# Kernel optimization log

Hardware: AMD Instinct MI355X
Metric: run time of the kernel (lower is better)

The kernel has to match this reference:

```python
import jax, jax.numpy as jnp
import numpy as np

N = 30000      # nodes
E = 480000     # edges (avg degree 16)
NF = 4         # n_field
NM = 8         # n_meshfield
H = 128        # hidden_size == latent_size
T = 4          # n_time
DEPTH_MID = 8  # depth-2 middle convs per GCNBlock
EPS = 1e-5     # PyG InstanceNorm eps
DT = 5 * (4.0 / 200)  # = 0.1, hard-coded in forward


def _glorot(k, shape):
    fan_in = shape[-2]
    return (jax.random.uniform(k, shape, jnp.float32, -1.0, 1.0) / np.sqrt(fan_in)).astype(jnp.float32)


def setup_inputs() -> dict:
    key = jax.random.key(0)
    ks = jax.random.split(key, 12)
    inp = {}
    inp['F_0'] = jax.random.normal(ks[0], (N, NF), jnp.float32)
    inp['edge_index'] = jax.random.randint(ks[1], (2, E), 0, N)
    inp['meshfield'] = jax.random.normal(ks[2], (N, NM), jnp.float32)
    inp['n_time'] = T
    # mesh_decriptor GCNBlock params (10 GCNConv layers)
    inp['mesh_W0'] = _glorot(ks[3], (NM, H)); inp['mesh_b0'] = jnp.zeros((H,), jnp.float32)
    inp['mesh_Wh'] = _glorot(ks[4], (DEPTH_MID, H, H)); inp['mesh_bh'] = jnp.zeros((DEPTH_MID, H), jnp.float32)
    inp['mesh_W9'] = _glorot(ks[5], (H, H)); inp['mesh_b9'] = jnp.zeros((H,), jnp.float32)
    # differentiator GCNBlock params; input dim = n_field + latent_size
    din = NF + H
    inp['diff_W0'] = _glorot(ks[6], (din, H)); inp['diff_b0'] = jnp.zeros((H,), jnp.float32)
    inp['diff_Wh'] = _glorot(ks[7], (DEPTH_MID, H, H)); inp['diff_bh'] = jnp.zeros((DEPTH_MID, H), jnp.float32)
    inp['diff_W9'] = _glorot(ks[8], (H, NF)); inp['diff_b9'] = jnp.zeros((NF,), jnp.float32)
    return inp


def _gcn_norm(edge_index, n):
    # PyG GCNConv: add self-loops, sym-normalize D^-1/2 (A+I) D^-1/2
    loops = jnp.arange(n)
    row = jnp.concatenate([edge_index[0], loops])
    col = jnp.concatenate([edge_index[1], loops])
    deg = jax.ops.segment_sum(jnp.ones_like(col, jnp.float32), col, num_segments=n)
    dinv = jnp.where(deg > 0, jax.lax.rsqrt(jnp.maximum(deg, 1.0)), 0.0)
    return row, col, dinv[row] * dinv[col]


def _conv(x, W, b, row, col, enorm, n):
    h = x @ W                                   # [n, out]
    m = h[row] * enorm[:, None]                 # gather + edge normalization
    return jax.ops.segment_sum(m, col, num_segments=n) + b  # scatter-add + bias


def _instance_norm(x):
    # single graph, affine=False: per-channel normalize over nodes
    m = x.mean(axis=0)
    v = x.var(axis=0)
    return (x - m) * jax.lax.rsqrt(v + EPS)


def _gcn_block(x, W0, b0, Wh, bh, W9, b9, row, col, enorm, n):
    x = _conv(x, W0, b0, row, col, enorm, n)
    x = _instance_norm(x)
    def body(c, wb):
        W, b = wb
        return _conv(jax.nn.relu(c), W, b, row, col, enorm, n), None
    x, _ = jax.lax.scan(body, x, (Wh, bh))
    return _conv(x, W9, b9, row, col, enorm, n)


def reference(F_0, edge_index, meshfield, n_time,
              mesh_W0, mesh_b0, mesh_Wh, mesh_bh, mesh_W9, mesh_b9,
              diff_W0, diff_b0, diff_Wh, diff_bh, diff_W9, diff_b9):
    n = F_0.shape[0]
    row, col, enorm = _gcn_norm(edge_index, n)
    mesh = jnp.tanh(_gcn_block(meshfield, mesh_W0, mesh_b0, mesh_Wh, mesh_bh,
                               mesh_W9, mesh_b9, row, col, enorm, n))

    def step(F_cur, _):
        x = jnp.concatenate([F_cur, mesh], axis=1)   # [n, n_field + latent]
        F_dot = jnp.tanh(_gcn_block(x, diff_W0, diff_b0, diff_Wh, diff_bh,
                                    diff_W9, diff_b9, row, col, enorm, n))
        F_next = jnp.tanh(F_cur + F_dot * DT)
        # original: F_current = F_next.detach()
        return jax.lax.stop_gradient(F_next), (F_next, F_dot)

    _, (Fs, F_dots) = jax.lax.scan(step, F_0, None, length=n_time)
    # [T, n, f] -> [n, T, f] to match torch.cat(..., dim=1)
    return jnp.transpose(Fs, (1, 0, 2)), jnp.transpose(F_dots, (1, 0, 2))
```

## Files before the change

kernel.cpp:

```cpp
#include <hip/hip_runtime.h>
#include <math.h>

typedef __attribute__((ext_vector_type(8))) short short8;
typedef __attribute__((ext_vector_type(4))) float f32x4;
typedef unsigned int uint;
typedef unsigned short ushort;

__device__ __forceinline__ ushort f2bf(float f) {
  union { float f; uint u; } v; v.f = f;
  uint u = v.u;
  uint r = (u + 0x7FFFu + ((u >> 16) & 1u)) >> 16;
  return (ushort)r;
}
__device__ __forceinline__ float bflo(uint u) { union { uint u; float f; } v; v.u = u << 16; return v.f; }
__device__ __forceinline__ float bfhi(uint u) { union { uint u; float f; } v; v.u = u & 0xFFFF0000u; return v.f; }
__device__ __forceinline__ uint packbf(float a, float b) { return (uint)f2bf(a) | ((uint)f2bf(b) << 16); }


static __global__ void k_count(const int* __restrict__ col, int* __restrict__ cnt, int E) {
  int e = blockIdx.x * blockDim.x + threadIdx.x;
  if (e < E) atomicAdd(&cnt[col[e]], 1);
}

static __global__ void k_dinv(const int* __restrict__ cnt, float* __restrict__ dinv, int N) {
  int v = blockIdx.x * blockDim.x + threadIdx.x;
  if (v < N) dinv[v] = rsqrtf((float)cnt[v] + 1.0f);
}

static __global__ void k_scan(const int* __restrict__ cnt, int* __restrict__ rowptr, int N) {
  __shared__ int buf[1024];
  __shared__ int carry;
  int t = threadIdx.x;
  if (t == 0) carry = 0;
  __syncthreads();
  for (int base = 0; base < N; base += 1024) {
    int i = base + t;
    int x = (i < N) ? cnt[i] : 0;
    buf[t] = x;
    __syncthreads();
    for (int o = 1; o < 1024; o <<= 1) {
      int val = (t >= o) ? buf[t - o] : 0;
      __syncthreads();
      buf[t] += val;
      __syncthreads();
    }
    int inc = buf[t];
    if (i < N) rowptr[i] = carry + inc - x;
    __syncthreads();
    if (t == 1023) carry += inc;
    __syncthreads();
  }
  if (t == 0) rowptr[N] = carry;
}

static __global__ void k_fill(const int* __restrict__ row, const int* __restrict__ col,
                              const float* __restrict__ dinv, const int* __restrict__ rowptr,
                              int* __restrict__ fillc, int* __restrict__ csr_src,
                              float* __restrict__ csr_w, int E) {
  int e = blockIdx.x * blockDim.x + threadIdx.x;
  if (e >= E) return;
  int s = row[e], d = col[e];
  int pos = rowptr[d] + atomicAdd(&fillc[d], 1);
  csr_src[pos] = s;
  csr_w[pos] = dinv[s] * dinv[d];
}


static __global__ void k_wprep(const float* __restrict__ W, ushort* __restrict__ Wt,
                               int K, int Kpad, int Nc) {
  int l = blockIdx.y;
  int idx = blockIdx.x * 256 + threadIdx.x;
  if (idx >= Nc * Kpad) return;
  int n = idx / Kpad, k = idx - n * Kpad;
  const float* Wl = W + (size_t)l * K * Nc;
  ushort* Wtl = Wt + (size_t)l * Nc * Kpad;
  Wtl[idx] = (k < K) ? f2bf(Wl[(size_t)k * Nc + n]) : (ushort)0;
}


static __global__ __launch_bounds__(256) void k_gemm16(
    const ushort* __restrict__ A, const ushort* __restrict__ Bt,
    ushort* __restrict__ Y, int M, int K) {
  __shared__ ushort As[128 * 40];
  __shared__ ushort Bs[128 * 40];
  const int tid = threadIdx.x;
  const int lane = tid & 63;
  const int wave = tid >> 6;
  const int wr = wave >> 1, wc = wave & 1;
  const int bm = blockIdx.x * 128;
  const int l15 = lane & 15, lk = lane >> 4;
  const int r0 = tid >> 2, o0 = tid & 3;

  f32x4 acc[4][4];
#pragma unroll
  for (int i = 0; i < 4; ++i)
#pragma unroll
    for (int j = 0; j < 4; ++j) acc[i][j] = (f32x4){0.f, 0.f, 0.f, 0.f};

  for (int k0 = 0; k0 < K; k0 += 32) {
    short8 a0 = *(const short8*)(A + (size_t)(bm + r0) * K + k0 + o0 * 8);
    short8 a1 = *(const short8*)(A + (size_t)(bm + r0 + 64) * K + k0 + o0 * 8);
    short8 b0 = *(const short8*)(Bt + (size_t)r0 * K + k0 + o0 * 8);
    short8 b1 = *(const short8*)(Bt + (size_t)(r0 + 64) * K + k0 + o0 * 8);
    __syncthreads();
    *(short8*)(As + r0 * 40 + o0 * 8) = a0;
    *(short8*)(As + (r0 + 64) * 40 + o0 * 8) = a1;
    *(short8*)(Bs + r0 * 40 + o0 * 8) = b0;
    *(short8*)(Bs + (r0 + 64) * 40 + o0 * 8) = b1;
    __syncthreads();
    short8 af[4], bfr[4];
#pragma unroll
    for (int i = 0; i < 4; ++i) {
      af[i]  = *(const short8*)(As + (wr * 64 + i * 16 + l15) * 40 + lk * 8);
      bfr[i] = *(const short8*)(Bs + (wc * 64 + i * 16 + l15) * 40 + lk * 8);
    }
#pragma unroll
    for (int i = 0; i < 4; ++i)
#pragma unroll
      for (int j = 0; j < 4; ++j)
        acc[i][j] = __builtin_amdgcn_mfma_f32_16x16x32_bf16(af[i], bfr[j], acc[i][j], 0, 0, 0);
  }
#pragma unroll
  for (int i = 0; i < 4; ++i) {
#pragma unroll
    for (int r = 0; r < 4; ++r) {
      int row = bm + wr * 64 + i * 16 + lk * 4 + r;
      if (row < M) {
#pragma unroll
        for (int j = 0; j < 4; ++j) {
          int col = wc * 64 + j * 16 + l15;
          Y[(size_t)row * 128 + col] = f2bf(acc[i][j][r]);
        }
      }
    }
  }
}


static __global__ __launch_bounds__(256) void k_gemm_small(
    const ushort* __restrict__ A, const float* __restrict__ W, float* __restrict__ Y, int M) {
  __shared__ float Ws[512];
  int tid = threadIdx.x;
  for (int i = tid; i < 512; i += 256) Ws[i] = W[i];
  __syncthreads();
  int m = blockIdx.x * 256 + tid;
  if (m >= M) return;
  const uint* a = (const uint*)(A + (size_t)m * 128);
  float a0 = 0, a1 = 0, a2 = 0, a3 = 0;
#pragma unroll 8
  for (int k2 = 0; k2 < 64; ++k2) {
    uint u = a[k2];
    float x0 = bflo(u), x1 = bfhi(u);
    const float* w = Ws + k2 * 8;
    a0 += x0 * w[0] + x1 * w[4];
    a1 += x0 * w[1] + x1 * w[5];
    a2 += x0 * w[2] + x1 * w[6];
    a3 += x0 * w[3] + x1 * w[7];
  }
  float* y = Y + (size_t)m * 4;
  y[0] = a0; y[1] = a1; y[2] = a2; y[3] = a3;
}


static __global__ __launch_bounds__(256) void k_agg16(
    const ushort* __restrict__ Hm, const int* __restrict__ rowptr,
    const int* __restrict__ csr_src, const float* __restrict__ csr_w,
    const float* __restrict__ dinv, const float* __restrict__ bias,
    float* __restrict__ outF, int actF,
    ushort* __restrict__ outB, int reluB,
    int N) {
  int node = blockIdx.x * 4 + (threadIdx.x >> 6);
  if (node >= N) return;
  int lane = threadIdx.x & 63;
  const uint* __restrict__ Hu = (const uint*)Hm;
  float dv = dinv[node];
  float w = dv * dv;
  uint su = Hu[(size_t)node * 64 + lane];
  float acc0 = w * bflo(su), acc1 = w * bfhi(su);
  int s = rowptr[node], e = rowptr[node + 1];
  int i = s;
  for (; i + 4 <= e; i += 4) {
    int s0 = csr_src[i], s1 = csr_src[i + 1], s2 = csr_src[i + 2], s3 = csr_src[i + 3];
    float w0 = csr_w[i], w1 = csr_w[i + 1], w2 = csr_w[i + 2], w3 = csr_w[i + 3];
    uint u0 = Hu[(size_t)s0 * 64 + lane];
    uint u1 = Hu[(size_t)s1 * 64 + lane];
    uint u2 = Hu[(size_t)s2 * 64 + lane];
    uint u3 = Hu[(size_t)s3 * 64 + lane];
    acc0 += w0 * bflo(u0) + w1 * bflo(u1) + w2 * bflo(u2) + w3 * bflo(u3);
    acc1 += w0 * bfhi(u0) + w1 * bfhi(u1) + w2 * bfhi(u2) + w3 * bfhi(u3);
  }
  for (; i < e; ++i) {
    int s0 = csr_src[i];
    float w0 = csr_w[i];
    uint u0 = Hu[(size_t)s0 * 64 + lane];
    acc0 += w0 * bflo(u0);
    acc1 += w0 * bfhi(u0);
  }
  float2 bb = *(const float2*)(bias + lane * 2);
  acc0 += bb.x; acc1 += bb.y;
  if (outF) {
    float o0 = acc0, o1 = acc1;
    if (actF == 2) { o0 = tanhf(o0); o1 = tanhf(o1); }
    *(float2*)(outF + (size_t)node * 128 + lane * 2) = make_float2(o0, o1);
  }
  if (outB) {
    float o0 = acc0, o1 = acc1;
    if (reluB) { o0 = fmaxf(o0, 0.f); o1 = fmaxf(o1, 0.f); }
    ((uint*)outB)[(size_t)node * 64 + lane] = packbf(o0, o1);
  }
}


static __global__ void k_agg_f32(const float* __restrict__ Hm, float* __restrict__ Y,
                                 const int* __restrict__ rowptr, const int* __restrict__ csr_src,
                                 const float* __restrict__ csr_w, const float* __restrict__ dinv,
                                 const float* __restrict__ bias, int N, int C) {
  int idx = blockIdx.x * blockDim.x + threadIdx.x;
  if (idx >= N * C) return;
  int v = idx / C, c = idx - v * C;
  float dv = dinv[v];
  float acc = dv * dv * Hm[(size_t)v * C + c];
  int s = rowptr[v], e = rowptr[v + 1];
  for (int i = s; i < e; ++i) acc += csr_w[i] * Hm[(size_t)csr_src[i] * C + c];
  Y[idx] = acc + bias[c];
}


static __global__ __launch_bounds__(256) void k_in_part(const float* __restrict__ X,
                                                        float* __restrict__ acc, int N) {
  int tid = threadIdx.x;
  int c4 = (tid & 31) * 4;
  int rsub = tid >> 5;
  int row0 = blockIdx.x * 512 + rsub;
  int rowEnd = min(blockIdx.x * 512 + 512, N);
  float s0 = 0, s1 = 0, s2 = 0, s3 = 0, q0 = 0, q1 = 0, q2 = 0, q3 = 0;
  for (int r = row0; r < rowEnd; r += 8) {
    float4 v = *(const float4*)(X + (size_t)r * 128 + c4);
    s0 += v.x; s1 += v.y; s2 += v.z; s3 += v.w;
    q0 += v.x * v.x; q1 += v.y * v.y; q2 += v.z * v.z; q3 += v.w * v.w;
  }
  __shared__ float sb[8][132], qb[8][132];
  sb[rsub][c4] = s0; sb[rsub][c4 + 1] = s1; sb[rsub][c4 + 2] = s2; sb[rsub][c4 + 3] = s3;
  qb[rsub][c4] = q0; qb[rsub][c4 + 1] = q1; qb[rsub][c4 + 2] = q2; qb[rsub][c4 + 3] = q3;
  __syncthreads();
  if (tid < 128) {
    float ss = 0, qq = 0;
#pragma unroll
    for (int g = 0; g < 8; ++g) { ss += sb[g][tid]; qq += qb[g][tid]; }
    atomicAdd(&acc[tid], ss);
    atomicAdd(&acc[128 + tid], qq);
  }
}

static __global__ void k_in_fin(const float* __restrict__ acc, float* __restrict__ meanv,
                                float* __restrict__ scalev, int N) {
  int c = threadIdx.x;
  if (c < 128) {
    float m = acc[c] / (float)N;
    float var = acc[128 + c] / (float)N - m * m;
    meanv[c] = m;
    scalev[c] = rsqrtf(var + 1e-5f);
  }
}

static __global__ void k_in_apply(const float* __restrict__ X, const float* __restrict__ meanv,
                                  const float* __restrict__ scalev, ushort* __restrict__ outB, int N) {
  int idx = blockIdx.x * blockDim.x + threadIdx.x;
  if (idx >= N * 64) return;
  int c2 = idx & 63;
  float2 x = *(const float2*)(X + (size_t)idx * 2);
  float2 mm = *(const float2*)(meanv + c2 * 2);
  float2 sc = *(const float2*)(scalev + c2 * 2);
  float o0 = fmaxf((x.x - mm.x) * sc.x, 0.f);
  float o1 = fmaxf((x.y - mm.y) * sc.y, 0.f);
  ((uint*)outB)[idx] = packbf(o0, o1);
}


static __global__ void k_cast_mesh0(const float* __restrict__ MF, ushort* __restrict__ A16, int N) {
  int idx = blockIdx.x * blockDim.x + threadIdx.x;
  if (idx >= N * 16) return;
  int v = idx >> 4, c2 = idx & 15;
  int c = c2 * 2;
  float x0 = 0.f, x1 = 0.f;
  if (c < 8) { x0 = MF[v * 8 + c]; x1 = MF[v * 8 + c + 1]; }
  ((uint*)A16)[idx] = packbf(x0, x1);
}

static __global__ void k_concat16(const float* __restrict__ F, const float* __restrict__ meshL,
                                  ushort* __restrict__ A16, int N) {
  int idx = blockIdx.x * blockDim.x + threadIdx.x;
  if (idx >= N * 80) return;
  int v = idx / 80, c2 = idx - v * 80;
  int c = c2 * 2;
  float x0 = 0.f, x1 = 0.f;
  if (c < 4) { x0 = F[v * 4 + c]; x1 = F[v * 4 + c + 1]; }
  else if (c < 132) { float2 m = *(const float2*)(meshL + (size_t)v * 128 + (c - 4)); x0 = m.x; x1 = m.y; }
  ((uint*)A16)[idx] = packbf(x0, x1);
}

static __global__ void k_copy(const float* __restrict__ A, float* __restrict__ B, int n) {
  int i = blockIdx.x * blockDim.x + threadIdx.x;
  if (i < n) B[i] = A[i];
}

static __global__ void k_step_finish(const float* __restrict__ fdot_pre,
                                     const float* __restrict__ Fcur, float* __restrict__ Fnext,
                                     float* __restrict__ out, int N, int T, int t) {
  int idx = blockIdx.x * blockDim.x + threadIdx.x;
  if (idx >= N * 4) return;
  int v = idx >> 2, f = idx & 3;
  float fd = tanhf(fdot_pre[idx]);
  float fn = tanhf(Fcur[idx] + fd * 0.1f);
  Fnext[idx] = fn;
  out[((size_t)v * T + t) * 4 + f] = fn;
  out[(size_t)N * T * 4 + ((size_t)v * T + t) * 4 + f] = fd;
}


extern "C" void kernel_launch(void* const* d_in, const int* in_sizes, int n_in,
                              void* d_out, int out_size, void* d_ws, size_t ws_size,
                              hipStream_t stream) {
  const float* F0        = (const float*)d_in[0];
  const int*   ei        = (const int*)d_in[1];
  const float* meshfield = (const float*)d_in[2];
  const float* mesh_W0 = (const float*)d_in[4];
  const float* mesh_b0 = (const float*)d_in[5];
  const float* mesh_Wh = (const float*)d_in[6];
  const float* mesh_bh = (const float*)d_in[7];
  const float* mesh_W9 = (const float*)d_in[8];
  const float* mesh_b9 = (const float*)d_in[9];
  const float* diff_W0 = (const float*)d_in[10];
  const float* diff_b0 = (const float*)d_in[11];
  const float* diff_Wh = (const float*)d_in[12];
  const float* diff_bh = (const float*)d_in[13];
  const float* diff_W9 = (const float*)d_in[14];
  const float* diff_b9 = (const float*)d_in[15];

  const int N = in_sizes[0] / 4;
  const int E = in_sizes[1] / 2;
  const int H = in_sizes[5];
  const int T = out_size / (N * 4 * 2);
  const int DEPTH = in_sizes[7] / H;
  const int Mpad = (N + 127) / 128 * 128;
  const int DIN_K = 160;

  const int* erow = ei;
  const int* ecol = ei + E;

  char* p = (char*)d_ws;
  auto alloc = [&](size_t bytes) { char* r = p; p += (bytes + 255) & ~(size_t)255; return r; };
  float* dinv   = (float*)alloc((size_t)N * 4);
  float* X      = (float*)alloc((size_t)N * H * 4);
  float* meshL  = (float*)alloc((size_t)N * H * 4);
  ushort* A16   = (ushort*)alloc((size_t)Mpad * DIN_K * 2);
  ushort* Msg16 = (ushort*)alloc((size_t)Mpad * H * 2);
  float* msg4   = (float*)alloc((size_t)N * 4 * 4);
  float* fdotp  = (float*)alloc((size_t)N * 4 * 4);
  float* fcur0  = (float*)alloc((size_t)N * 4 * 4);
  float* fcur1  = (float*)alloc((size_t)N * 4 * 4);
  float* statac = (float*)alloc(256 * 4);
  float* meanv  = (float*)alloc(128 * 4);
  float* scalev = (float*)alloc(128 * 4);
  ushort* W0t_m = (ushort*)alloc((size_t)128 * 32 * 2);
  ushort* Wht_m = (ushort*)alloc((size_t)DEPTH * 128 * 128 * 2);
  ushort* W9t_m = (ushort*)alloc((size_t)128 * 128 * 2);
  ushort* W0t_d = (ushort*)alloc((size_t)128 * 160 * 2);
  ushort* Wht_d = (ushort*)alloc((size_t)DEPTH * 128 * 128 * 2);
  float* csr_w  = (float*)alloc((size_t)E * 4);
  int* cnt      = (int*)alloc((size_t)N * 4);
  int* rowptr   = (int*)alloc((size_t)(N + 1) * 4);
  int* fillc    = (int*)alloc((size_t)N * 4);
  int* csr_src  = (int*)alloc((size_t)E * 4);

  {
    dim3 g0((128 * 32 + 255) / 256, 1);
    k_wprep<<<g0, 256, 0, stream>>>(mesh_W0, W0t_m, 8, 32, 128);
    dim3 gh((128 * 128 + 255) / 256, DEPTH);
    k_wprep<<<gh, 256, 0, stream>>>(mesh_Wh, Wht_m, 128, 128, 128);
    dim3 g9((128 * 128 + 255) / 256, 1);
    k_wprep<<<g9, 256, 0, stream>>>(mesh_W9, W9t_m, 128, 128, 128);
    dim3 gd((128 * 160 + 255) / 256, 1);
    k_wprep<<<gd, 256, 0, stream>>>(diff_W0, W0t_d, 132, 160, 128);
    k_wprep<<<gh, 256, 0, stream>>>(diff_Wh, Wht_d, 128, 128, 128);
  }

  hipMemsetAsync(cnt, 0, (size_t)N * 4, stream);
  hipMemsetAsync(fillc, 0, (size_t)N * 4, stream);
  k_count<<<(E + 255) / 256, 256, 0, stream>>>(ecol, cnt, E);
  k_dinv<<<(N + 255) / 256, 256, 0, stream>>>(cnt, dinv, N);
  k_scan<<<1, 1024, 0, stream>>>(cnt, rowptr, N);
  k_fill<<<(E + 255) / 256, 256, 0, stream>>>(erow, ecol, dinv, rowptr, fillc, csr_src, csr_w, E);

  auto gemm = [&](const ushort* A, const ushort* Bt, int K) {
    k_gemm16<<<Mpad / 128, 256, 0, stream>>>(A, Bt, Msg16, N, K);
  };
  auto agg = [&](const float* bias, float* outF, int actF, ushort* outB, int reluB) {
    k_agg16<<<(N + 3) / 4, 256, 0, stream>>>(Msg16, rowptr, csr_src, csr_w, dinv, bias,
                                             outF, actF, outB, reluB, N);
  };
  auto instnorm = [&]() {
    hipMemsetAsync(statac, 0, 256 * 4, stream);
    k_in_part<<<(N + 511) / 512, 256, 0, stream>>>(X, statac, N);
    k_in_fin<<<1, 128, 0, stream>>>(statac, meanv, scalev, N);
    k_in_apply<<<(N * 64 + 255) / 256, 256, 0, stream>>>(X, meanv, scalev, A16, N);
  };

  k_cast_mesh0<<<(N * 16 + 255) / 256, 256, 0, stream>>>(meshfield, A16, N);
  gemm(A16, W0t_m, 32);
  agg(mesh_b0, X, 0, nullptr, 0);
  instnorm();
  for (int i = 0; i < DEPTH; ++i) {
    gemm(A16, Wht_m + (size_t)i * 128 * 128, 128);
    agg(mesh_bh + (size_t)i * H, nullptr, 0, A16, (i < DEPTH - 1) ? 1 : 0);
  }
  gemm(A16, W9t_m, 128);
  agg(mesh_b9, meshL, 2 , nullptr, 0);

  k_copy<<<(N * 4 + 255) / 256, 256, 0, stream>>>(F0, fcur0, N * 4);
  float* fc = fcur0;
  float* fn = fcur1;
  float* out = (float*)d_out;

  for (int t = 0; t < T; ++t) {
    k_concat16<<<(N * 80 + 255) / 256, 256, 0, stream>>>(fc, meshL, A16, N);
    gemm(A16, W0t_d, DIN_K);
    agg(diff_b0, X, 0, nullptr, 0);
    instnorm();
    for (int i = 0; i < DEPTH; ++i) {
      gemm(A16, Wht_d + (size_t)i * 128 * 128, 128);
      agg(diff_bh + (size_t)i * H, nullptr, 0, A16, (i < DEPTH - 1) ? 1 : 0);
    }
    k_gemm_small<<<(N + 255) / 256, 256, 0, stream>>>(A16, diff_W9, msg4, N);
    k_agg_f32<<<(N * 4 + 255) / 256, 256, 0, stream>>>(msg4, fdotp, rowptr, csr_src, csr_w,
                                                       dinv, diff_b9, N, 4);
    k_step_finish<<<(N * 4 + 255) / 256, 256, 0, stream>>>(fdotp, fc, fn, out, N, T, t);
    float* tmp = fc; fc = fn; fn = tmp;
  }
}
```

Before: 2.092 ms.

## Reorder first differentiator conv to aggregate before GEMM and restructure helpers

The first differentiator conv now aggregates its inputs before the matmul (A(XW) = (AX)W). The mesh-latent aggregation is computed once outside the time loop, and only the 4-field part is re-aggregated each step. This removes one 128-wide gather/scatter aggregation per time step. The change also replaces the serial block scan with a per-thread-chunk warp scan, replaces the atomic instance-norm reductions with per-block partial sums, adds an 8-way unrolled aggregation loop, and uses ping-pong activation buffers. The mesh latent is stored as bf16 rather than fp32, and the bias is applied after the aggregation/GEMM swap, which slightly changes rounding.

```diff
diff --git a/kernel.cpp b/kernel.cpp
--- a/kernel.cpp
+++ b/kernel.cpp
@@ -27,30 +27,39 @@
   if (v < N) dinv[v] = rsqrtf((float)cnt[v] + 1.0f);
 }
 
-static __global__ void k_scan(const int* __restrict__ cnt, int* __restrict__ rowptr, int N) {
-  __shared__ int buf[1024];
-  __shared__ int carry;
-  int t = threadIdx.x;
-  if (t == 0) carry = 0;
+static __global__ __launch_bounds__(1024) void k_scan(const int* __restrict__ cnt,
+                                                      int* __restrict__ rowptr, int N) {
+  const int t = threadIdx.x;
+  const int per = (N + 1023) / 1024;
+  int lo = t * per, hi = min(lo + per, N);
+  if (lo > N) lo = N;
+  if (hi < lo) hi = lo;
+  int sum = 0;
+  for (int i = lo; i < hi; ++i) sum += cnt[i];
+  int lane = t & 63, w = t >> 6;
+  int v = sum;
+#pragma unroll
+  for (int d = 1; d < 64; d <<= 1) {
+    int u = __shfl_up(v, d, 64);
+    if (lane >= d) v += u;
+  }
+  __shared__ int wsum[16];
+  if (lane == 63) wsum[w] = v;
   __syncthreads();
-  for (int base = 0; base < N; base += 1024) {
-    int i = base + t;
-    int x = (i < N) ? cnt[i] : 0;
-    buf[t] = x;
-    __syncthreads();
-    for (int o = 1; o < 1024; o <<= 1) {
-      int val = (t >= o) ? buf[t - o] : 0;
-      __syncthreads();
-      buf[t] += val;
-      __syncthreads();
+  if (t < 16) {
+    int x = wsum[t];
+#pragma unroll
+    for (int d = 1; d < 16; d <<= 1) {
+      int u = __shfl_up(x, d, 64);
+      if (t >= d) x += u;
     }
-    int inc = buf[t];
-    if (i < N) rowptr[i] = carry + inc - x;
-    __syncthreads();
-    if (t == 1023) carry += inc;
-    __syncthreads();
-  }
-  if (t == 0) rowptr[N] = carry;
+    wsum[t] = x;
+  }
+  __syncthreads();
+  int base = (w ? wsum[w - 1] : 0) + v - sum;
+  int run = base;
+  for (int i = lo; i < hi; ++i) { rowptr[i] = run; run += cnt[i]; }
+  if (t == 1023) rowptr[N] = run;
 }
 
 static __global__ void k_fill(const int* __restrict__ row, const int* __restrict__ col,
@@ -80,7 +89,9 @@
 
 static __global__ __launch_bounds__(256) void k_gemm16(
     const ushort* __restrict__ A, const ushort* __restrict__ Bt,
-    ushort* __restrict__ Y, int M, int K) {
+    int K, const float* __restrict__ bias,
+    float* __restrict__ outF, ushort* __restrict__ outB,
+    int M) {
   __shared__ ushort As[128 * 40];
   __shared__ ushort Bs[128 * 40];
   const int tid = threadIdx.x;
@@ -125,12 +136,13 @@
 #pragma unroll
     for (int r = 0; r < 4; ++r) {
       int row = bm + wr * 64 + i * 16 + lk * 4 + r;
-      if (row < M) {
-#pragma unroll
-        for (int j = 0; j < 4; ++j) {
-          int col = wc * 64 + j * 16 + l15;
-          Y[(size_t)row * 128 + col] = f2bf(acc[i][j][r]);
-        }
+      if (row >= M) continue;
+#pragma unroll
+      for (int j = 0; j < 4; ++j) {
+        int col = wc * 64 + j * 16 + l15;
+        float v = acc[i][j][r] + (bias ? bias[col] : 0.f);
+        if (outF) outF[(size_t)row * 128 + col] = v;
+        if (outB) outB[(size_t)row * 128 + col] = f2bf(v);
       }
     }
   }
@@ -166,8 +178,8 @@
     const ushort* __restrict__ Hm, const int* __restrict__ rowptr,
     const int* __restrict__ csr_src, const float* __restrict__ csr_w,
     const float* __restrict__ dinv, const float* __restrict__ bias,
-    float* __restrict__ outF, int actF,
-    ushort* __restrict__ outB, int reluB,
+    float* __restrict__ outF,
+    ushort* __restrict__ outB, int actB,
     int N) {
   int node = blockIdx.x * 4 + (threadIdx.x >> 6);
   if (node >= N) return;
@@ -179,6 +191,24 @@
   float acc0 = w * bflo(su), acc1 = w * bfhi(su);
   int s = rowptr[node], e = rowptr[node + 1];
   int i = s;
+  for (; i + 8 <= e; i += 8) {
+    int s0 = csr_src[i], s1 = csr_src[i + 1], s2 = csr_src[i + 2], s3 = csr_src[i + 3];
+    int s4 = csr_src[i + 4], s5 = csr_src[i + 5], s6 = csr_src[i + 6], s7 = csr_src[i + 7];
+    float w0 = csr_w[i], w1 = csr_w[i + 1], w2 = csr_w[i + 2], w3 = csr_w[i + 3];
+    float w4 = csr_w[i + 4], w5 = csr_w[i + 5], w6 = csr_w[i + 6], w7 = csr_w[i + 7];
+    uint u0 = Hu[(size_t)s0 * 64 + lane];
+    uint u1 = Hu[(size_t)s1 * 64 + lane];
+    uint u2 = Hu[(size_t)s2 * 64 + lane];
+    uint u3 = Hu[(size_t)s3 * 64 + lane];
+    uint u4 = Hu[(size_t)s4 * 64 + lane];
+    uint u5 = Hu[(size_t)s5 * 64 + lane];
+    uint u6 = Hu[(size_t)s6 * 64 + lane];
+    uint u7 = Hu[(size_t)s7 * 64 + lane];
+    acc0 += w0 * bflo(u0) + w1 * bflo(u1) + w2 * bflo(u2) + w3 * bflo(u3)
+          + w4 * bflo(u4) + w5 * bflo(u5) + w6 * bflo(u6) + w7 * bflo(u7);
+    acc1 += w0 * bfhi(u0) + w1 * bfhi(u1) + w2 * bfhi(u2) + w3 * bfhi(u3)
+          + w4 * bfhi(u4) + w5 * bfhi(u5) + w6 * bfhi(u6) + w7 * bfhi(u7);
+  }
   for (; i + 4 <= e; i += 4) {
     int s0 = csr_src[i], s1 = csr_src[i + 1], s2 = csr_src[i + 2], s3 = csr_src[i + 3];
     float w0 = csr_w[i], w1 = csr_w[i + 1], w2 = csr_w[i + 2], w3 = csr_w[i + 3];
@@ -196,18 +226,52 @@
     acc0 += w0 * bflo(u0);
     acc1 += w0 * bfhi(u0);
   }
-  float2 bb = *(const float2*)(bias + lane * 2);
-  acc0 += bb.x; acc1 += bb.y;
+  if (bias) {
+    float2 bb = *(const float2*)(bias + lane * 2);
+    acc0 += bb.x; acc1 += bb.y;
+  }
   if (outF) {
-    float o0 = acc0, o1 = acc1;
-    if (actF == 2) { o0 = tanhf(o0); o1 = tanhf(o1); }
-    *(float2*)(outF + (size_t)node * 128 + lane * 2) = make_float2(o0, o1);
+    *(float2*)(outF + (size_t)node * 128 + lane * 2) = make_float2(acc0, acc1);
   }
   if (outB) {
     float o0 = acc0, o1 = acc1;
-    if (reluB) { o0 = fmaxf(o0, 0.f); o1 = fmaxf(o1, 0.f); }
+    if (actB == 1) { o0 = fmaxf(o0, 0.f); o1 = fmaxf(o1, 0.f); }
+    else if (actB == 2) { o0 = tanhf(o0); o1 = tanhf(o1); }
     ((uint*)outB)[(size_t)node * 64 + lane] = packbf(o0, o1);
   }
+}
+
+
+static __global__ void k_aggF(const float* __restrict__ F, const int* __restrict__ rowptr,
+                              const int* __restrict__ csr_src, const float* __restrict__ csr_w,
+                              const float* __restrict__ dinv, ushort* __restrict__ AggF16, int N) {
+  int idx = blockIdx.x * blockDim.x + threadIdx.x;
+  if (idx >= N * 2) return;
+  int v = idx >> 1, pr = idx & 1;
+  float dv = dinv[v];
+  float2 x = *(const float2*)(F + (size_t)v * 4 + pr * 2);
+  float a0 = dv * dv * x.x, a1 = dv * dv * x.y;
+  int s = rowptr[v], e = rowptr[v + 1];
+  for (int i = s; i < e; ++i) {
+    float2 xs = *(const float2*)(F + (size_t)csr_src[i] * 4 + pr * 2);
+    float w = csr_w[i];
+    a0 += w * xs.x;
+    a1 += w * xs.y;
+  }
+  ((uint*)AggF16)[idx] = packbf(a0, a1);
+}
+
+
+static __global__ void k_concat160(const ushort* __restrict__ AggF16,
+                                   const ushort* __restrict__ AggMesh16,
+                                   ushort* __restrict__ C160, int N) {
+  int idx = blockIdx.x * blockDim.x + threadIdx.x;
+  if (idx >= N * 80) return;
+  int v = idx / 80, j = idx - v * 80;
+  uint val = 0;
+  if (j < 2) val = ((const uint*)AggF16)[(size_t)v * 2 + j];
+  else if (j < 66) val = ((const uint*)AggMesh16)[(size_t)v * 64 + (j - 2)];
+  ((uint*)C160)[idx] = val;
 }
 
 
@@ -227,7 +291,7 @@
 
 
 static __global__ __launch_bounds__(256) void k_in_part(const float* __restrict__ X,
-                                                        float* __restrict__ acc, int N) {
+                                                        float* __restrict__ partial, int N) {
   int tid = threadIdx.x;
   int c4 = (tid & 31) * 4;
   int rsub = tid >> 5;
@@ -247,20 +311,24 @@
     float ss = 0, qq = 0;
 #pragma unroll
     for (int g = 0; g < 8; ++g) { ss += sb[g][tid]; qq += qb[g][tid]; }
-    atomicAdd(&acc[tid], ss);
-    atomicAdd(&acc[128 + tid], qq);
-  }
-}
-
-static __global__ void k_in_fin(const float* __restrict__ acc, float* __restrict__ meanv,
-                                float* __restrict__ scalev, int N) {
+    partial[(size_t)blockIdx.x * 256 + tid] = ss;
+    partial[(size_t)blockIdx.x * 256 + 128 + tid] = qq;
+  }
+}
+
+static __global__ void k_in_fin(const float* __restrict__ partial, int NB,
+                                float* __restrict__ meanv, float* __restrict__ scalev, int N) {
   int c = threadIdx.x;
-  if (c < 128) {
-    float m = acc[c] / (float)N;
-    float var = acc[128 + c] / (float)N - m * m;
-    meanv[c] = m;
-    scalev[c] = rsqrtf(var + 1e-5f);
-  }
+  if (c >= 128) return;
+  float s = 0, q = 0;
+  for (int b = 0; b < NB; ++b) {
+    s += partial[(size_t)b * 256 + c];
+    q += partial[(size_t)b * 256 + 128 + c];
+  }
+  float m = s / (float)N;
+  float var = q / (float)N - m * m;
+  meanv[c] = m;
+  scalev[c] = rsqrtf(var + 1e-5f);
 }
 
 static __global__ void k_in_apply(const float* __restrict__ X, const float* __restrict__ meanv,
@@ -277,26 +345,14 @@
 }
 
 
-static __global__ void k_cast_mesh0(const float* __restrict__ MF, ushort* __restrict__ A16, int N) {
+static __global__ void k_cast_mesh0(const float* __restrict__ MF, ushort* __restrict__ C32, int N) {
   int idx = blockIdx.x * blockDim.x + threadIdx.x;
   if (idx >= N * 16) return;
   int v = idx >> 4, c2 = idx & 15;
   int c = c2 * 2;
   float x0 = 0.f, x1 = 0.f;
   if (c < 8) { x0 = MF[v * 8 + c]; x1 = MF[v * 8 + c + 1]; }
-  ((uint*)A16)[idx] = packbf(x0, x1);
-}
-
-static __global__ void k_concat16(const float* __restrict__ F, const float* __restrict__ meshL,
-                                  ushort* __restrict__ A16, int N) {
-  int idx = blockIdx.x * blockDim.x + threadIdx.x;
-  if (idx >= N * 80) return;
-  int v = idx / 80, c2 = idx - v * 80;
-  int c = c2 * 2;
-  float x0 = 0.f, x1 = 0.f;
-  if (c < 4) { x0 = F[v * 4 + c]; x1 = F[v * 4 + c + 1]; }
-  else if (c < 132) { float2 m = *(const float2*)(meshL + (size_t)v * 128 + (c - 4)); x0 = m.x; x1 = m.y; }
-  ((uint*)A16)[idx] = packbf(x0, x1);
+  ((uint*)C32)[idx] = packbf(x0, x1);
 }
 
 static __global__ void k_copy(const float* __restrict__ A, float* __restrict__ B, int n) {
@@ -343,35 +399,40 @@
   const int T = out_size / (N * 4 * 2);
   const int DEPTH = in_sizes[7] / H;
   const int Mpad = (N + 127) / 128 * 128;
-  const int DIN_K = 160;
+  const int NB_IN = (N + 511) / 512;
 
   const int* erow = ei;
   const int* ecol = ei + E;
 
   char* p = (char*)d_ws;
   auto alloc = [&](size_t bytes) { char* r = p; p += (bytes + 255) & ~(size_t)255; return r; };
-  float* dinv   = (float*)alloc((size_t)N * 4);
-  float* X      = (float*)alloc((size_t)N * H * 4);
-  float* meshL  = (float*)alloc((size_t)N * H * 4);
-  ushort* A16   = (ushort*)alloc((size_t)Mpad * DIN_K * 2);
-  ushort* Msg16 = (ushort*)alloc((size_t)Mpad * H * 2);
-  float* msg4   = (float*)alloc((size_t)N * 4 * 4);
-  float* fdotp  = (float*)alloc((size_t)N * 4 * 4);
-  float* fcur0  = (float*)alloc((size_t)N * 4 * 4);
-  float* fcur1  = (float*)alloc((size_t)N * 4 * 4);
-  float* statac = (float*)alloc(256 * 4);
-  float* meanv  = (float*)alloc(128 * 4);
-  float* scalev = (float*)alloc(128 * 4);
-  ushort* W0t_m = (ushort*)alloc((size_t)128 * 32 * 2);
-  ushort* Wht_m = (ushort*)alloc((size_t)DEPTH * 128 * 128 * 2);
-  ushort* W9t_m = (ushort*)alloc((size_t)128 * 128 * 2);
-  ushort* W0t_d = (ushort*)alloc((size_t)128 * 160 * 2);
-  ushort* Wht_d = (ushort*)alloc((size_t)DEPTH * 128 * 128 * 2);
-  float* csr_w  = (float*)alloc((size_t)E * 4);
-  int* cnt      = (int*)alloc((size_t)N * 4);
-  int* rowptr   = (int*)alloc((size_t)(N + 1) * 4);
-  int* fillc    = (int*)alloc((size_t)N * 4);
-  int* csr_src  = (int*)alloc((size_t)E * 4);
+  float* dinv     = (float*)alloc((size_t)N * 4);
+  float* X        = (float*)alloc((size_t)N * H * 4);
+  ushort* C32     = (ushort*)alloc((size_t)Mpad * 32 * 2);
+  ushort* C160    = (ushort*)alloc((size_t)Mpad * 160 * 2);
+  ushort* X16a    = (ushort*)alloc((size_t)Mpad * 128 * 2);
+  ushort* X16b    = (ushort*)alloc((size_t)Mpad * 128 * 2);
+  ushort* Msg16   = (ushort*)alloc((size_t)Mpad * 128 * 2);
+  ushort* meshL16 = (ushort*)alloc((size_t)Mpad * 128 * 2);
+  ushort* AggM16  = (ushort*)alloc((size_t)Mpad * 128 * 2);
+  ushort* AggF16  = (ushort*)alloc((size_t)Mpad * 4 * 2);
+  float* msg4     = (float*)alloc((size_t)N * 4 * 4);
+  float* fdotp    = (float*)alloc((size_t)N * 4 * 4);
+  float* fcur0    = (float*)alloc((size_t)N * 4 * 4);
+  float* fcur1    = (float*)alloc((size_t)N * 4 * 4);
+  float* partial  = (float*)alloc((size_t)NB_IN * 256 * 4);
+  float* meanv    = (float*)alloc(128 * 4);
+  float* scalev   = (float*)alloc(128 * 4);
+  ushort* W0t_m   = (ushort*)alloc((size_t)128 * 32 * 2);
+  ushort* Wht_m   = (ushort*)alloc((size_t)DEPTH * 128 * 128 * 2);
+  ushort* W9t_m   = (ushort*)alloc((size_t)128 * 128 * 2);
+  ushort* W0t_d   = (ushort*)alloc((size_t)128 * 160 * 2);
+  ushort* Wht_d   = (ushort*)alloc((size_t)DEPTH * 128 * 128 * 2);
+  float* csr_w    = (float*)alloc((size_t)E * 4);
+  int* cnt        = (int*)alloc((size_t)N * 4);
+  int* rowptr     = (int*)alloc((size_t)(N + 1) * 4);
+  int* fillc      = (int*)alloc((size_t)N * 4);
+  int* csr_src    = (int*)alloc((size_t)E * 4);
 
   {
     dim3 g0((128 * 32 + 255) / 256, 1);
@@ -392,30 +453,35 @@
   k_scan<<<1, 1024, 0, stream>>>(cnt, rowptr, N);
   k_fill<<<(E + 255) / 256, 256, 0, stream>>>(erow, ecol, dinv, rowptr, fillc, csr_src, csr_w, E);
 
-  auto gemm = [&](const ushort* A, const ushort* Bt, int K) {
-    k_gemm16<<<Mpad / 128, 256, 0, stream>>>(A, Bt, Msg16, N, K);
+  auto gemm = [&](const ushort* A, const ushort* Bt, int K, const float* bias,
+                  float* oF, ushort* oB) {
+    k_gemm16<<<Mpad / 128, 256, 0, stream>>>(A, Bt, K, bias, oF, oB, N);
   };
-  auto agg = [&](const float* bias, float* outF, int actF, ushort* outB, int reluB) {
-    k_agg16<<<(N + 3) / 4, 256, 0, stream>>>(Msg16, rowptr, csr_src, csr_w, dinv, bias,
-                                             outF, actF, outB, reluB, N);
+  auto agg = [&](const ushort* Hm, const float* bias, float* oF, ushort* oB, int actB) {
+    k_agg16<<<(N + 3) / 4, 256, 0, stream>>>(Hm, rowptr, csr_src, csr_w, dinv, bias,
+                                             oF, oB, actB, N);
   };
   auto instnorm = [&]() {
-    hipMemsetAsync(statac, 0, 256 * 4, stream);
-    k_in_part<<<(N + 511) / 512, 256, 0, stream>>>(X, statac, N);
-    k_in_fin<<<1, 128, 0, stream>>>(statac, meanv, scalev, N);
-    k_in_apply<<<(N * 64 + 255) / 256, 256, 0, stream>>>(X, meanv, scalev, A16, N);
+    k_in_part<<<NB_IN, 256, 0, stream>>>(X, partial, N);
+    k_in_fin<<<1, 128, 0, stream>>>(partial, NB_IN, meanv, scalev, N);
+    k_in_apply<<<(N * 64 + 255) / 256, 256, 0, stream>>>(X, meanv, scalev, X16a, N);
   };
 
-  k_cast_mesh0<<<(N * 16 + 255) / 256, 256, 0, stream>>>(meshfield, A16, N);
-  gemm(A16, W0t_m, 32);
-  agg(mesh_b0, X, 0, nullptr, 0);
+  k_cast_mesh0<<<(N * 16 + 255) / 256, 256, 0, stream>>>(meshfield, C32, N);
+  gemm(C32, W0t_m, 32, nullptr, nullptr, Msg16);
+  agg(Msg16, mesh_b0, X, nullptr, 0);
   instnorm();
-  for (int i = 0; i < DEPTH; ++i) {
-    gemm(A16, Wht_m + (size_t)i * 128 * 128, 128);
-    agg(mesh_bh + (size_t)i * H, nullptr, 0, A16, (i < DEPTH - 1) ? 1 : 0);
-  }
-  gemm(A16, W9t_m, 128);
-  agg(mesh_b9, meshL, 2 , nullptr, 0);
+  {
+    ushort* cur = X16a; ushort* nxt = X16b;
+    for (int i = 0; i < DEPTH; ++i) {
+      gemm(cur, Wht_m + (size_t)i * 128 * 128, 128, nullptr, nullptr, Msg16);
+      agg(Msg16, mesh_bh + (size_t)i * H, nullptr, nxt, (i < DEPTH - 1) ? 1 : 0);
+      ushort* tmp = cur; cur = nxt; nxt = tmp;
+    }
+    gemm(cur, W9t_m, 128, nullptr, nullptr, Msg16);
+    agg(Msg16, mesh_b9, nullptr, meshL16, 2 );
+  }
+  agg(meshL16, nullptr, nullptr, AggM16, 0);
 
   k_copy<<<(N * 4 + 255) / 256, 256, 0, stream>>>(F0, fcur0, N * 4);
   float* fc = fcur0;
@@ -423,15 +489,17 @@
   float* out = (float*)d_out;
 
   for (int t = 0; t < T; ++t) {
-    k_concat16<<<(N * 80 + 255) / 256, 256, 0, stream>>>(fc, meshL, A16, N);
-    gemm(A16, W0t_d, DIN_K);
-    agg(diff_b0, X, 0, nullptr, 0);
+    k_aggF<<<(N * 2 + 255) / 256, 256, 0, stream>>>(fc, rowptr, csr_src, csr_w, dinv, AggF16, N);
+    k_concat160<<<(N * 80 + 255) / 256, 256, 0, stream>>>(AggF16, AggM16, C160, N);
+    gemm(C160, W0t_d, 160, diff_b0, X, nullptr);
     instnorm();
+    ushort* cur = X16a; ushort* nxt = X16b;
     for (int i = 0; i < DEPTH; ++i) {
-      gemm(A16, Wht_d + (size_t)i * 128 * 128, 128);
-      agg(diff_bh + (size_t)i * H, nullptr, 0, A16, (i < DEPTH - 1) ? 1 : 0);
+      gemm(cur, Wht_d + (size_t)i * 128 * 128, 128, nullptr, nullptr, Msg16);
+      agg(Msg16, diff_bh + (size_t)i * H, nullptr, nxt, (i < DEPTH - 1) ? 1 : 0);
+      ushort* tmp = cur; cur = nxt; nxt = tmp;
     }
-    k_gemm_small<<<(N + 255) / 256, 256, 0, stream>>>(A16, diff_W9, msg4, N);
+    k_gemm_small<<<(N + 255) / 256, 256, 0, stream>>>(cur, diff_W9, msg4, N);
     k_agg_f32<<<(N * 4 + 255) / 256, 256, 0, stream>>>(msg4, fdotp, rowptr, csr_src, csr_w,
                                                        dinv, diff_b9, N, 4);
     k_step_finish<<<(N * 4 + 255) / 256, 256, 0, stream>>>(fdotp, fc, fn, out, N, T, t);
```

Result: slower. 2.170 ms (+3.7%).
